# Optimization experiments

Measured on AMD Instinct MI355X. Metric: run time of the kernel, lower is better.

Reference implementation:

```python
import jax, jax.numpy as jnp
from jax import lax
import numpy as np

B = 512       # number of sequences
L = 512       # max_seq_length
A = 20        # amino-acid alphabet / input_size
C = 8         # conv channels
N_REST = 8    # total_layers - 1 extra conv+pool blocks (log2(512)=9)
STD = 0.01    # non-trainable self.std


def setup_inputs() -> dict:
    key = jax.random.key(0)
    k1, k2, k3, k4 = jax.random.split(key, 4)
    # one-hot residue encoding, as the nonzero()-based scatters assume
    aa = jax.random.randint(k1, (B, L), 0, A)
    x = jax.nn.one_hot(aa, A, dtype=jnp.float32)          # (B, L, 20)
    masks = jnp.ones((B, L), dtype=jnp.float32)           # unused by forward
    # BLOSUM-like integer substitution matrix
    blosum = jax.random.randint(k2, (A, A), -4, 12).astype(jnp.float32)
    blosum = (blosum + blosum.T) / 2.0
    lpm = blosum                                          # trainable copy
    pm = jnp.clip(blosum, 0.0, None)                      # clamped buffer
    w_first = jax.random.normal(k3, (C, 1, 3), dtype=jnp.float32) * 0.3
    w_rest = jax.random.normal(k4, (N_REST, C, C, 3), dtype=jnp.float32) * 0.2
    return {"x": x, "masks": masks, "lpm": lpm, "pm": pm,
            "w_first": w_first, "w_rest": w_rest}


def _column(xp, lpm, pm):
    # xp: (B, 20, L). For each nonzero (b,i,p), the torch loops write
    # value(i->k) at (b,k,p): k=i+1..18 uses lpm[i,k]*pm[i,k];
    # k=0..i-1 uses lpm[k,i]*pm[k,i]; column k=19 and diag never written.
    nz = (xp != 0).astype(xp.dtype)
    prod = jnp.clip(lpm, 1e-3, 1.0) * pm                  # (20,20)
    i = jnp.arange(A)[:, None]
    k = jnp.arange(A)[None, :]
    V = jnp.where(k > i, prod, jnp.where(k < i, prod.T, 0.0))
    V = V.at[:, A - 1].set(0.0)                           # k=19 never written
    return jnp.einsum('bip,ik->bkp', nz, V)


def _row(xp):
    # Gaussian-decay neighbor writes at p +/- d (d=1,2,3), indices clamped
    # to [0, L-1]; later (larger-d) index_put calls overwrite earlier ones.
    nz = (xp != 0).astype(xp.dtype)
    ar = jnp.arange(L)
    new_x = jnp.zeros_like(xp)
    for d in (1, 2, 3):
        val = jnp.exp(jnp.asarray(-(d * d) / (2.0 * STD * STD), xp.dtype))
        up = jnp.zeros_like(nz).at[:, :, jnp.clip(ar + d, 0, L - 1)].max(nz)
        dn = jnp.zeros_like(nz).at[:, :, jnp.clip(ar - d, 0, L - 1)].max(nz)
        new_x = jnp.where(jnp.maximum(up, dn) > 0, val, new_x)
    return new_x


def _convs(h, w_first, w_rest):
    dn = ('NCH', 'OIH', 'NCH')
    h = lax.conv_general_dilated(h, w_first, (1,), ((1, 1),),
                                 dimension_numbers=dn)
    h = h.reshape(h.shape[0], h.shape[1], -1, 2).mean(-1)   # AvgPool1d(2)
    for li in range(N_REST):
        h = lax.conv_general_dilated(h, w_rest[li], (1,), ((1, 1),),
                                     dimension_numbers=dn)
        h = h.reshape(h.shape[0], h.shape[1], -1, 2).mean(-1)
    return h  # (N, C, 1)


def reference(x, masks, lpm, pm, w_first, w_rest):
    seq_num = x.shape[0]
    xp = jnp.transpose(x, (0, 2, 1))                        # (B, 20, L)
    xp = xp + _column(xp, lpm, pm) + _row(xp)
    h = xp.reshape(seq_num * A, 1, L)
    h = _convs(h, w_first, w_rest)                          # (B*20, 8, 1)
    return h.squeeze(-1).reshape(seq_num, A, -1)            # (B, 20, 8)
```

## Files before the change

kernel.cpp:

```cpp
#include <hip/hip_runtime.h>


__global__ void build_U(const float* __restrict__ lpm,
                        const float* __restrict__ pm,
                        float* __restrict__ U){
    int t = threadIdx.x;
    for (int idx = t; idx < 400; idx += 64){
        int i = idx / 20, k = idx % 20;
        float v = 0.f;
        if (k != 19 && k != i){
            int r = (k > i) ? i : k;
            int c = (k > i) ? k : i;
            float l = fminf(fmaxf(lpm[r*20 + c], 1e-3f), 1.0f);
            v = l * pm[r*20 + c];
        }
        U[idx] = v + ((i == k) ? 1.0f : 0.0f);
    }
}

__global__ __launch_bounds__(64) void build_Weff(
        const float* __restrict__ wf,
        const float* __restrict__ wr,
        float* __restrict__ Weff){
    int p = blockIdx.x;
    int t = threadIdx.x;
    __shared__ float s[512];
    __shared__ float bufA[8*256];
    __shared__ float bufB[8*128];
    __shared__ float taps[8*8*4];

    for (int j = t; j < 512; j += 64) s[j] = (j == p) ? 1.f : 0.f;
    if (t < 8){
        float w0 = wf[t*3+0], w1 = wf[t*3+1], w2 = wf[t*3+2];
        taps[t*4+0] = 0.5f*w0;
        taps[t*4+1] = 0.5f*(w0+w1);
        taps[t*4+2] = 0.5f*(w1+w2);
        taps[t*4+3] = 0.5f*w2;
    }
    __syncthreads();
    for (int idx = t; idx < 8*256; idx += 64){
        int c = idx >> 8, q = idx & 255;
        int j = 2*q;
        float sm1 = (j >= 1) ? s[j-1] : 0.f;
        float s0 = s[j];
        float s1 = s[j+1];
        float s2 = (j+2 < 512) ? s[j+2] : 0.f;
        const float* tp = &taps[c*4];
        bufA[c*256 + q] = tp[0]*sm1 + tp[1]*s0 + tp[2]*s1 + tp[3]*s2;
    }
    __syncthreads();
    float* inb  = bufA;
    float* outb = bufB;
    int Ln = 256, lsh = 7;
    for (int l = 0; l < 8; l++){
        {
            int c = t >> 3, ci = t & 7;
            const float* w = wr + ((l*8 + c)*8 + ci)*3;
            float w0 = w[0], w1 = w[1], w2 = w[2];
            taps[t*4+0] = 0.5f*w0;
            taps[t*4+1] = 0.5f*(w0+w1);
            taps[t*4+2] = 0.5f*(w1+w2);
            taps[t*4+3] = 0.5f*w2;
        }
        __syncthreads();
        int Lo = Ln >> 1;
        for (int idx = t; idx < 8*Lo; idx += 64){
            int c = idx >> lsh, q = idx & (Lo-1);
            int j = 2*q;
            float acc = 0.f;
            #pragma unroll
            for (int ci = 0; ci < 8; ci++){
                const float* tp = &taps[(c*8+ci)*4];
                const float* h = &inb[ci*Ln];
                float hm1 = (j >= 1) ? h[j-1] : 0.f;
                float h0  = h[j];
                float h1  = h[j+1];
                float h2  = (j+2 < Ln) ? h[j+2] : 0.f;
                acc += tp[0]*hm1 + tp[1]*h0 + tp[2]*h1 + tp[3]*h2;
            }
            outb[c*Lo + q] = acc;
        }
        __syncthreads();
        float* tmp = inb; inb = outb; outb = tmp;
        Ln = Lo; lsh -= 1;
    }
    if (t < 8) Weff[t*512 + p] = inb[t];
}

__global__ __launch_bounds__(256) void cnn_main(
        const float* __restrict__ x,
        const float* __restrict__ Weff,
        const float* __restrict__ U,
        float* __restrict__ out){
    int b = blockIdx.x;
    int t = threadIdx.x;
    __shared__ float W[8*512];
    __shared__ float Us[400];
    __shared__ float T[160];
    for (int idx = t; idx < 4096; idx += 256) W[idx] = Weff[idx];
    for (int idx = t; idx < 400; idx += 256) Us[idx] = U[idx];
    if (t < 160) T[t] = 0.f;
    __syncthreads();
    const float* xb = x + (size_t)b * (512*20);
    for (int p = t; p < 512; p += 256){
        const float4* f4 = (const float4*)(xb + p*20);
        int aa = 0;
        #pragma unroll
        for (int j = 0; j < 5; j++){
            float4 v = f4[j];
            if (v.x != 0.f) aa = 4*j + 0;
            if (v.y != 0.f) aa = 4*j + 1;
            if (v.z != 0.f) aa = 4*j + 2;
            if (v.w != 0.f) aa = 4*j + 3;
        }
        #pragma unroll
        for (int c = 0; c < 8; c++){
            atomicAdd(&T[c*20 + aa], W[c*512 + p]);
        }
    }
    __syncthreads();
    if (t < 160){
        int k = t >> 3, c = t & 7;
        float acc = 0.f;
        #pragma unroll
        for (int i = 0; i < 20; i++) acc += T[c*20 + i] * Us[i*20 + k];
        out[(size_t)b*160 + t] = acc;
    }
}

extern "C" void kernel_launch(void* const* d_in, const int* in_sizes, int n_in,
                              void* d_out, int out_size, void* d_ws, size_t ws_size,
                              hipStream_t stream){
    const float* x   = (const float*)d_in[0];
    const float* lpm = (const float*)d_in[2];
    const float* pm  = (const float*)d_in[3];
    const float* wf  = (const float*)d_in[4];
    const float* wr  = (const float*)d_in[5];
    float* Weff = (float*)d_ws;
    float* U    = Weff + 8*512;

    hipLaunchKernelGGL(build_U,    dim3(1),   dim3(64),  0, stream, lpm, pm, U);
    hipLaunchKernelGGL(build_Weff, dim3(512), dim3(64),  0, stream, wf, wr, Weff);
    hipLaunchKernelGGL(cnn_main,   dim3(512), dim3(256), 0, stream, x, Weff, U,
                       (float*)d_out);
}
```

Baseline: 111.4 us.

## Compute Weff impulse response over sliding window, fold U into main kernel

build_Weff now propagates the unit impulse through the conv/pool stack using only an 8-wide window per channel around the impulse's receptive field, instead of full-length buffers at every layer. This removes most of the per-block arithmetic and shared-memory traffic. The build_U kernel is removed and the substitution matrix is computed inline in cnn_main, which saves one launch but repeats the lpm/pm loads and clamps in every block. Per-wavefront partial histograms cut contention on the shared-memory atomics, at the cost of an extra reduction step and an extra barrier.

Result: faster. 98.16 us (-11.9%).

```diff
diff --git a/kernel.cpp b/kernel.cpp
--- a/kernel.cpp
+++ b/kernel.cpp
@@ -1,61 +1,37 @@
 #include <hip/hip_runtime.h>
 
-
-__global__ void build_U(const float* __restrict__ lpm,
-                        const float* __restrict__ pm,
-                        float* __restrict__ U){
-    int t = threadIdx.x;
-    for (int idx = t; idx < 400; idx += 64){
-        int i = idx / 20, k = idx % 20;
-        float v = 0.f;
-        if (k != 19 && k != i){
-            int r = (k > i) ? i : k;
-            int c = (k > i) ? k : i;
-            float l = fminf(fmaxf(lpm[r*20 + c], 1e-3f), 1.0f);
-            v = l * pm[r*20 + c];
-        }
-        U[idx] = v + ((i == k) ? 1.0f : 0.0f);
-    }
-}
 
 __global__ __launch_bounds__(64) void build_Weff(
         const float* __restrict__ wf,
         const float* __restrict__ wr,
         float* __restrict__ Weff){
-    int p = blockIdx.x;
-    int t = threadIdx.x;
-    __shared__ float s[512];
-    __shared__ float bufA[8*256];
-    __shared__ float bufB[8*128];
-    __shared__ float taps[8*8*4];
+    int p = blockIdx.x, t = threadIdx.x;
+    int c = t >> 3, u = t & 7;
+    __shared__ float winA[64];
+    __shared__ float winB[64];
+    __shared__ float taps[256];
 
-    for (int j = t; j < 512; j += 64) s[j] = (j == p) ? 1.f : 0.f;
-    if (t < 8){
-        float w0 = wf[t*3+0], w1 = wf[t*3+1], w2 = wf[t*3+2];
-        taps[t*4+0] = 0.5f*w0;
-        taps[t*4+1] = 0.5f*(w0+w1);
-        taps[t*4+2] = 0.5f*(w1+w2);
-        taps[t*4+3] = 0.5f*w2;
+    int base = (p >> 1) - 1; if (base < 0) base = 0;
+    {
+        float w0 = wf[c*3+0], w1 = wf[c*3+1], w2 = wf[c*3+2];
+        float tap0 = 0.5f*w0, tap1 = 0.5f*(w0+w1), tap2 = 0.5f*(w1+w2), tap3 = 0.5f*w2;
+        int q = base + u;
+        float v = 0.f;
+        if (q < 256){
+            int j = p - 2*q;
+            if (j == -1) v = tap0;
+            else if (j == 0) v = tap1;
+            else if (j == 1) v = tap2;
+            else if (j == 2) v = tap3;
+        }
+        winA[c*8+u] = v;
     }
-    __syncthreads();
-    for (int idx = t; idx < 8*256; idx += 64){
-        int c = idx >> 8, q = idx & 255;
-        int j = 2*q;
-        float sm1 = (j >= 1) ? s[j-1] : 0.f;
-        float s0 = s[j];
-        float s1 = s[j+1];
-        float s2 = (j+2 < 512) ? s[j+2] : 0.f;
-        const float* tp = &taps[c*4];
-        bufA[c*256 + q] = tp[0]*sm1 + tp[1]*s0 + tp[2]*s1 + tp[3]*s2;
-    }
-    __syncthreads();
-    float* inb  = bufA;
-    float* outb = bufB;
-    int Ln = 256, lsh = 7;
+    float* inw  = winA;
+    float* outw = winB;
+    int Ln = 256;
     for (int l = 0; l < 8; l++){
         {
-            int c = t >> 3, ci = t & 7;
-            const float* w = wr + ((l*8 + c)*8 + ci)*3;
+            const float* w = wr + ((l*8 + c)*8 + u)*3;
             float w0 = w[0], w1 = w[1], w2 = w[2];
             taps[t*4+0] = 0.5f*w0;
             taps[t*4+1] = 0.5f*(w0+w1);
@@ -64,44 +40,46 @@
         }
         __syncthreads();
         int Lo = Ln >> 1;
-        for (int idx = t; idx < 8*Lo; idx += 64){
-            int c = idx >> lsh, q = idx & (Lo-1);
-            int j = 2*q;
-            float acc = 0.f;
+        int nb = (base - 2) >> 1; if (nb < 0) nb = 0;
+        int q = nb + u;
+        float acc = 0.f;
+        if (q < Lo){
             #pragma unroll
             for (int ci = 0; ci < 8; ci++){
                 const float* tp = &taps[(c*8+ci)*4];
-                const float* h = &inb[ci*Ln];
-                float hm1 = (j >= 1) ? h[j-1] : 0.f;
-                float h0  = h[j];
-                float h1  = h[j+1];
-                float h2  = (j+2 < Ln) ? h[j+2] : 0.f;
-                acc += tp[0]*hm1 + tp[1]*h0 + tp[2]*h1 + tp[3]*h2;
+                #pragma unroll
+                for (int j = -1; j <= 2; j++){
+                    int m  = 2*q + j;
+                    int wi = m - base;
+                    float h = (m >= 0 && m < Ln && wi >= 0 && wi < 8)
+                              ? inw[ci*8 + wi] : 0.f;
+                    acc += tp[j+1] * h;
+                }
             }
-            outb[c*Lo + q] = acc;
         }
+        outw[c*8+u] = acc;
+        float* tmp = inw; inw = outw; outw = tmp;
+        base = nb; Ln = Lo;
         __syncthreads();
-        float* tmp = inb; inb = outb; outb = tmp;
-        Ln = Lo; lsh -= 1;
     }
-    if (t < 8) Weff[t*512 + p] = inb[t];
+    if (u == 0) Weff[c*512 + p] = inw[c*8 + 0];
 }
 
 __global__ __launch_bounds__(256) void cnn_main(
         const float* __restrict__ x,
         const float* __restrict__ Weff,
-        const float* __restrict__ U,
+        const float* __restrict__ lpm,
+        const float* __restrict__ pm,
         float* __restrict__ out){
-    int b = blockIdx.x;
-    int t = threadIdx.x;
-    __shared__ float W[8*512];
-    __shared__ float Us[400];
-    __shared__ float T[160];
+    int b = blockIdx.x, t = threadIdx.x;
+    __shared__ float W[4096];
+    __shared__ float T[4][160];
+    __shared__ float Ts[160];
     for (int idx = t; idx < 4096; idx += 256) W[idx] = Weff[idx];
-    for (int idx = t; idx < 400; idx += 256) Us[idx] = U[idx];
-    if (t < 160) T[t] = 0.f;
+    for (int idx = t; idx < 640; idx += 256) (&T[0][0])[idx] = 0.f;
     __syncthreads();
-    const float* xb = x + (size_t)b * (512*20);
+    const float* xb = x + (size_t)b * 10240;
+    int wid = t >> 6;
     for (int p = t; p < 512; p += 256){
         const float4* f4 = (const float4*)(xb + p*20);
         int aa = 0;
@@ -114,16 +92,25 @@
             if (v.w != 0.f) aa = 4*j + 3;
         }
         #pragma unroll
-        for (int c = 0; c < 8; c++){
-            atomicAdd(&T[c*20 + aa], W[c*512 + p]);
-        }
+        for (int c = 0; c < 8; c++)
+            atomicAdd(&T[wid][c*20 + aa], W[c*512 + p]);
     }
+    __syncthreads();
+    if (t < 160) Ts[t] = T[0][t] + T[1][t] + T[2][t] + T[3][t];
     __syncthreads();
     if (t < 160){
         int k = t >> 3, c = t & 7;
-        float acc = 0.f;
-        #pragma unroll
-        for (int i = 0; i < 20; i++) acc += T[c*20 + i] * Us[i*20 + k];
+        float acc = Ts[c*20 + k];
+        if (k != 19){
+            #pragma unroll
+            for (int i = 0; i < 20; i++){
+                if (i == k) continue;
+                int r  = (i < k) ? i : k;
+                int cc = (i < k) ? k : i;
+                float l = fminf(fmaxf(lpm[r*20 + cc], 1e-3f), 1.0f);
+                acc += Ts[c*20 + i] * (l * pm[r*20 + cc]);
+            }
+        }
         out[(size_t)b*160 + t] = acc;
     }
 }
@@ -137,10 +124,8 @@
     const float* wf  = (const float*)d_in[4];
     const float* wr  = (const float*)d_in[5];
     float* Weff = (float*)d_ws;
-    float* U    = Weff + 8*512;
 
-    hipLaunchKernelGGL(build_U,    dim3(1),   dim3(64),  0, stream, lpm, pm, U);
     hipLaunchKernelGGL(build_Weff, dim3(512), dim3(64),  0, stream, wf, wr, Weff);
-    hipLaunchKernelGGL(cnn_main,   dim3(512), dim3(256), 0, stream, x, Weff, U,
+    hipLaunchKernelGGL(cnn_main,   dim3(512), dim3(256), 0, stream, x, Weff, lpm, pm,
                        (float*)d_out);
 }
```
